# Kernel optimization log

Measured on AMD Instinct MI355X. Metric: run time of the kernel, lower is better.

The kernel has to match this reference:

```python
import jax, jax.numpy as jnp
import numpy as np

T = 3072          # num tokens
HID = 5120        # hidden_size
H = 16            # num_local_heads
DN = 128          # qk_nope_head_dim
DR = 64           # qk_rope_head_dim
DQK = DN + DR     # qk_head_dim = 192
DV = 128          # v_head_dim
Q_RANK = 1536     # q_lora_rank
KV_RANK = 512     # kv_lora_rank


def rmsnorm(x, w, eps=1e-6):
    var = jnp.mean(jnp.square(x), axis=-1, keepdims=True)
    return x * jax.lax.rsqrt(var + eps) * w


def apply_rope(x, cos, sin):
    # neox-style rotate-half; x [..., DR], cos/sin broadcastable [..., DR//2]
    x1, x2 = jnp.split(x, 2, axis=-1)
    return jnp.concatenate([x1 * cos - x2 * sin, x2 * cos + x1 * sin], axis=-1)


def setup_inputs() -> dict:
    key = jax.random.key(0)
    ks = jax.random.split(key, 8)
    s = 0.02
    positions = jnp.arange(T, dtype=jnp.int32)
    hidden_states = jax.random.normal(ks[0], (T, HID), dtype=jnp.float32)
    llama_4_scaling = jnp.ones((T, 1, 1), dtype=jnp.float32)
    w_q_a = jax.random.normal(ks[1], (HID, Q_RANK), dtype=jnp.float32) * s
    q_a_ln_w = jnp.ones((Q_RANK,), dtype=jnp.float32)
    w_q_b = jax.random.normal(ks[2], (Q_RANK, H * DQK), dtype=jnp.float32) * s
    w_kv_a = jax.random.normal(ks[3], (HID, KV_RANK + DR), dtype=jnp.float32) * s
    kv_a_ln_w = jnp.ones((KV_RANK,), dtype=jnp.float32)
    w_kv_b = jax.random.normal(ks[4], (KV_RANK, H * (DN + DV)), dtype=jnp.float32) * s
    w_o = jax.random.normal(ks[5], (H * DV, HID), dtype=jnp.float32) * s
    # cos/sin cache: [max_pos, DR]; first half cos, second half sin
    inv_freq = 1.0 / (10000.0 ** (jnp.arange(0, DR, 2, dtype=jnp.float32) / DR))
    t = jnp.arange(T, dtype=jnp.float32)
    freqs = t[:, None] * inv_freq[None, :]              # [T, DR//2]
    cos_sin_cache = jnp.concatenate([jnp.cos(freqs), jnp.sin(freqs)], axis=-1)
    return {
        "positions": positions, "hidden_states": hidden_states,
        "llama_4_scaling": llama_4_scaling,
        "w_q_a": w_q_a, "q_a_ln_w": q_a_ln_w, "w_q_b": w_q_b,
        "w_kv_a": w_kv_a, "kv_a_ln_w": kv_a_ln_w, "w_kv_b": w_kv_b,
        "w_o": w_o, "cos_sin_cache": cos_sin_cache,
    }


def reference(positions, hidden_states, llama_4_scaling, w_q_a, q_a_ln_w,
              w_q_b, w_kv_a, kv_a_ln_w, w_kv_b, w_o, cos_sin_cache):
    # ---- Q path: low-rank down/up projection with RMSNorm ----
    q = rmsnorm(hidden_states @ w_q_a, q_a_ln_w) @ w_q_b       # [T, H*DQK]
    q = q.reshape(T, H, DQK)
    q_nope, q_pe = q[..., :DN], q[..., DN:]                    # [T,H,DN],[T,H,DR]

    # ---- KV path: compressed latent + shared rope key ----
    latent = hidden_states @ w_kv_a                            # [T, KV_RANK+DR]
    kv_a = rmsnorm(latent[:, :KV_RANK], kv_a_ln_w)             # [T, KV_RANK]
    k_pe = latent[:, KV_RANK:]                                 # [T, DR] (shared across heads)
    kv = (kv_a @ w_kv_b).reshape(T, H, DN + DV)
    k_nope, v = kv[..., :DN], kv[..., DN:]                     # [T,H,DN],[T,H,DV]

    # ---- partial RoPE on the rope slices only ----
    cs = cos_sin_cache[positions]                              # [T, DR]
    cos, sin = cs[:, :DR // 2], cs[:, DR // 2:]
    q_pe = apply_rope(q_pe, cos[:, None, :], sin[:, None, :])
    k_pe = apply_rope(k_pe, cos, sin)

    q = jnp.concatenate([q_nope, q_pe], axis=-1)               # [T, H, DQK]
    k = jnp.concatenate(
        [k_nope, jnp.broadcast_to(k_pe[:, None, :], (T, H, DR))], axis=-1)

    q = q * llama_4_scaling

    # ---- causal attention (v is zero-padded to DQK in the original;
    #      the pad contributes zeros and is sliced off, so we skip it) ----
    scale = 1.0 / jnp.sqrt(jnp.float32(DQK))
    scores = jnp.einsum('qhd,khd->hqk', q, k) * scale          # [H, T, T]
    causal = positions[:, None] >= positions[None, :]
    scores = jnp.where(causal[None, :, :], scores, jnp.finfo(scores.dtype).min)
    probs = jax.nn.softmax(scores, axis=-1)
    attn = jnp.einsum('hqk,khd->qhd', probs, v)                # [T, H, DV]

    return attn.reshape(T, H * DV) @ w_o                       # [T, HID]
```

## Files before the change

### kernel.cpp

```cpp
#include <hip/hip_runtime.h>
#include <hip/hip_bf16.h>
#include <math.h>

#define T_TOK 3072
#define HID_D 5120
#define NH 16
#define DN 128
#define DR 64
#define DQK 192
#define DV 128
#define QRANK 1536
#define KVRANK 512
#define MERGED_N 2176

typedef __attribute__((ext_vector_type(8))) short short8;
typedef __attribute__((ext_vector_type(4))) float f32x4;
typedef unsigned short u16;

__device__ __forceinline__ u16 f2bf(float f) {
    unsigned int u = __float_as_uint(f);
    unsigned int lsb = (u >> 16) & 1;
    u += 0x7fffu + lsb;
    return (u16)(u >> 16);
}
__device__ __forceinline__ float bf2f(u16 v) {
    return __uint_as_float(((unsigned int)v) << 16);
}

__device__ __forceinline__ void gload_lds16(const u16* g, u16* l) {
    __builtin_amdgcn_global_load_lds((const __attribute__((address_space(1))) void*)g,
                                     (__attribute__((address_space(3))) void*)l, 16, 0, 0);
}

__global__ __launch_bounds__(256) void convert_bf_k(const float* __restrict__ x,
                                                    u16* __restrict__ y, int n4)
{
    const int i = blockIdx.x * 256 + threadIdx.x;
    if (i < n4) {
        float4 v = ((const float4*)x)[i];
        ushort4 o;
        o.x = f2bf(v.x); o.y = f2bf(v.y); o.z = f2bf(v.z); o.w = f2bf(v.w);
        ((ushort4*)y)[i] = o;
    }
}

__global__ __launch_bounds__(256) void transpose_conv_k(const float* __restrict__ W,
                                                        u16* __restrict__ WT,
                                                        int K, int N)
{
    __shared__ float tile[32][33];
    const int n0 = blockIdx.x * 32, k0 = blockIdx.y * 32;
    const int tx = threadIdx.x & 31, ty = threadIdx.x >> 5;
#pragma unroll
    for (int i = 0; i < 32; i += 8) {
        const int nn = n0 + tx;
        tile[ty + i][tx] = (nn < N) ? W[(size_t)(k0 + ty + i) * N + nn] : 0.f;
    }
    __syncthreads();
#pragma unroll
    for (int i = 0; i < 32; i += 8) {
        WT[(size_t)(n0 + ty + i) * K + k0 + tx] = f2bf(tile[tx][ty + i]);
    }
}

template <bool BF16_OUT>
__global__ __launch_bounds__(256) void bgemm_bt_k(
    const u16* __restrict__ A, const u16* __restrict__ BT, void* __restrict__ C,
    int Nreal, int K, int lda, int ldb, int ldc)
{
    __shared__ __attribute__((aligned(16))) u16 As[128 * 32];
    __shared__ __attribute__((aligned(16))) u16 Bs[128 * 32];

    const int tid  = threadIdx.x;
    const int wave = tid >> 6, lane = tid & 63;
    const int quad = lane >> 4, l16 = lane & 15;
    const int wr = (wave >> 1) * 64, wc = (wave & 1) * 64;
    const int row0 = blockIdx.y * 128, col0 = blockIdx.x * 128;

    f32x4 acc[4][4];
#pragma unroll
    for (int i = 0; i < 4; ++i)
#pragma unroll
        for (int j = 0; j < 4; ++j) acc[i][j] = (f32x4){0.f, 0.f, 0.f, 0.f};

    const int sr  = tid >> 2;
    const int skc = (tid & 3) * 8;
    const u16* ap0 = A  + (size_t)(row0 + sr)      * lda + skc;
    const u16* ap1 = A  + (size_t)(row0 + sr + 64) * lda + skc;
    const u16* bp0 = BT + (size_t)(col0 + sr)      * ldb + skc;
    const u16* bp1 = BT + (size_t)(col0 + sr + 64) * ldb + skc;
    u16* al0 = As + tid * 8;
    u16* al1 = As + tid * 8 + 64 * 32;
    u16* bl0 = Bs + tid * 8;
    u16* bl1 = Bs + tid * 8 + 64 * 32;

    for (int kt = 0; kt < K; kt += 32) {
        gload_lds16(ap0 + kt, al0);
        gload_lds16(ap1 + kt, al1);
        gload_lds16(bp0 + kt, bl0);
        gload_lds16(bp1 + kt, bl1);
        __syncthreads();

        short8 af[4], bf[4];
#pragma unroll
        for (int mi = 0; mi < 4; ++mi)
            af[mi] = *(const short8*)(As + (wr + mi * 16 + l16) * 32 + quad * 8);
#pragma unroll
        for (int ni = 0; ni < 4; ++ni)
            bf[ni] = *(const short8*)(Bs + (wc + ni * 16 + l16) * 32 + quad * 8);
#pragma unroll
        for (int mi = 0; mi < 4; ++mi)
#pragma unroll
            for (int ni = 0; ni < 4; ++ni)
                acc[mi][ni] = __builtin_amdgcn_mfma_f32_16x16x32_bf16(
                    af[mi], bf[ni], acc[mi][ni], 0, 0, 0);
        __syncthreads();
    }

#pragma unroll
    for (int mi = 0; mi < 4; ++mi) {
#pragma unroll
        for (int ni = 0; ni < 4; ++ni) {
            const int col_g = col0 + wc + ni * 16 + l16;
            if (col_g < Nreal) {
#pragma unroll
                for (int r = 0; r < 4; ++r) {
                    const int row_g = row0 + wr + mi * 16 + quad * 4 + r;
                    if (BF16_OUT)
                        ((u16*)C)[(size_t)row_g * ldc + col_g] = f2bf(acc[mi][ni][r]);
                    else
                        ((float*)C)[(size_t)row_g * ldc + col_g] = acc[mi][ni][r];
                }
            }
        }
    }
}

__global__ __launch_bounds__(256) void rmsnorm_bf_k(const u16* __restrict__ x,
                                                    const float* __restrict__ w,
                                                    u16* __restrict__ y,
                                                    int width, int stride, int off)
{
    const int row = blockIdx.x;
    const u16* xr = x + (size_t)row * stride + off;
    float ss = 0.f;
    for (int i = threadIdx.x; i < width; i += 256) {
        float v = bf2f(xr[i]);
        ss += v * v;
    }
    __shared__ float red[256];
    red[threadIdx.x] = ss;
    __syncthreads();
    for (int s = 128; s > 0; s >>= 1) {
        if (threadIdx.x < s) red[threadIdx.x] += red[threadIdx.x + s];
        __syncthreads();
    }
    const float scale = rsqrtf(red[0] / (float)width + 1e-6f);
    for (int i = threadIdx.x; i < width; i += 256)
        y[(size_t)row * width + i] = f2bf(bf2f(xr[i]) * scale * w[i]);
}

__global__ void rope_scale_q_bf_k(const u16* __restrict__ q, const int* __restrict__ positions,
                                  const float* __restrict__ scaling,
                                  const float* __restrict__ cs_cache, u16* __restrict__ qb)
{
    const int t = blockIdx.x;
    const int pos = positions[t];
    const float* cs = cs_cache + (size_t)pos * DR;
    const float s = scaling[t];
    __shared__ float c_sh[32], s_sh[32];
    if (threadIdx.x < 32) {
        c_sh[threadIdx.x] = cs[threadIdx.x];
        s_sh[threadIdx.x] = cs[32 + threadIdx.x];
    }
    __syncthreads();
    const int tid = threadIdx.x;
    for (int h = 0; h < NH; ++h) {
        const u16* qr = q + ((size_t)t * NH + h) * DQK;
        u16* qo = qb + ((size_t)t * NH + h) * DQK;
        if (tid < 128) {
            qo[tid] = f2bf(bf2f(qr[tid]) * s);
        } else if (tid < 160) {
            const int d = tid - 128;
            const float x1 = bf2f(qr[128 + d]), x2 = bf2f(qr[160 + d]);
            qo[128 + d] = f2bf((x1 * c_sh[d] - x2 * s_sh[d]) * s);
            qo[160 + d] = f2bf((x2 * c_sh[d] + x1 * s_sh[d]) * s);
        }
    }
}

__global__ void rope_k_bf_k(const u16* __restrict__ qa_lat, u16* __restrict__ kpe,
                            const int* __restrict__ positions,
                            const float* __restrict__ cs_cache)
{
    const int t = blockIdx.x;
    const int d = threadIdx.x;
    if (d >= 32) return;
    const int pos = positions[t];
    const float* cs = cs_cache + (size_t)pos * DR;
    const float c = cs[d], sn = cs[32 + d];
    const u16* lr = qa_lat + (size_t)t * MERGED_N + QRANK + KVRANK;
    const float x1 = bf2f(lr[d]), x2 = bf2f(lr[32 + d]);
    kpe[(size_t)t * DR + d]      = f2bf(x1 * c - x2 * sn);
    kpe[(size_t)t * DR + 32 + d] = f2bf(x2 * c + x1 * sn);
}

__global__ __launch_bounds__(256) void transpose_v_k(const u16* __restrict__ kvb,
                                                     u16* __restrict__ vt)
{
    __shared__ u16 tile[64][72];
    const int t0 = blockIdx.x * 64, d0 = blockIdx.y * 64, h = blockIdx.z;
    const int tid = threadIdx.x;
    for (int cc = tid; cc < 64 * 8; cc += 256) {
        const int row = cc >> 3, c = (cc & 7) * 8;
        *(short8*)&tile[row][c] =
            *(const short8*)(kvb + ((size_t)(t0 + row) * NH + h) * (DN + DV) + DN + d0 + c);
    }
    __syncthreads();
    for (int cc = tid; cc < 64 * 8; cc += 256) {
        const int drow = cc >> 3, c = (cc & 7) * 8;
        short8 s;
#pragma unroll
        for (int j = 0; j < 8; ++j) s[j] = tile[c + j][drow];
        *(short8*)(vt + ((size_t)h * DV + d0 + drow) * T_TOK + t0 + c) = s;
    }
}

#define ATT_BM 128
#define ATT_BN 64
__global__ __launch_bounds__(512) void attn_mfma_k(
    const u16* __restrict__ qb, const u16* __restrict__ kvb,
    const u16* __restrict__ kpeb, const u16* __restrict__ vt,
    u16* __restrict__ attnb)
{
    __shared__ u16 Ks[ATT_BN][200];
    __shared__ u16 Vt[DV][72];
    __shared__ u16 Ps[8][16][72];

    const int tid  = threadIdx.x;
    const int wave = tid >> 6;
    const int lane = tid & 63;
    const int quad = lane >> 4;
    const int l16  = lane & 15;

    const int qblk = (int)gridDim.x - 1 - (int)blockIdx.x;
    const int h    = blockIdx.y;
    const int q0   = qblk * ATT_BM;
    const int wrow0 = q0 + wave * 16;
    const int qrow  = wrow0 + l16;

    short8 qf[6];
    {
        const u16* qp = qb + ((size_t)qrow * NH + h) * DQK + quad * 8;
#pragma unroll
        for (int c = 0; c < 6; ++c)
            qf[c] = *(const short8*)(qp + c * 32);
    }

    f32x4 oacc[8];
#pragma unroll
    for (int t = 0; t < 8; ++t) oacc[t] = (f32x4){0.f, 0.f, 0.f, 0.f};
    float m_old[4], l_run[4];
#pragma unroll
    for (int r = 0; r < 4; ++r) { m_old[r] = -1e30f; l_run[r] = 0.f; }

    const int nkt = (q0 + ATT_BM) / ATT_BN;
    for (int kt = 0; kt < nkt; ++kt) {
        const int k0 = kt * ATT_BN;
        __syncthreads();
        for (int cc = tid; cc < 64 * 24; cc += 512) {
            const int row = cc / 24, c = cc % 24;
            short8 v;
            if (c < 16) v = *(const short8*)(kvb + ((size_t)(k0 + row) * NH + h) * (DN + DV) + c * 8);
            else        v = *(const short8*)(kpeb + (size_t)(k0 + row) * DR + (c - 16) * 8);
            *(short8*)&Ks[row][c * 8] = v;
        }
        for (int cc = tid; cc < DV * 8; cc += 512) {
            const int row = cc >> 3, c = (cc & 7) * 8;
            *(short8*)&Vt[row][c] =
                *(const short8*)(vt + ((size_t)h * DV + row) * T_TOK + k0 + c);
        }
        __syncthreads();

        if (k0 <= wrow0 + 15) {
            f32x4 sacc[4];
#pragma unroll
            for (int t = 0; t < 4; ++t) sacc[t] = (f32x4){0.f, 0.f, 0.f, 0.f};
#pragma unroll
            for (int t = 0; t < 4; ++t) {
                const u16* kp = &Ks[t * 16 + l16][quad * 8];
#pragma unroll
                for (int c = 0; c < 6; ++c) {
                    short8 bfrag = *(const short8*)(kp + c * 32);
                    sacc[t] = __builtin_amdgcn_mfma_f32_16x16x32_bf16(qf[c], bfrag, sacc[t], 0, 0, 0);
                }
            }
            const float sc = 0.07216878364870322f;
            const int rbase = wrow0 + quad * 4;
            if (k0 + ATT_BN - 1 > wrow0) {
#pragma unroll
                for (int t = 0; t < 4; ++t) {
                    const int colg = k0 + t * 16 + l16;
#pragma unroll
                    for (int r = 0; r < 4; ++r) {
                        const float s = sacc[t][r] * sc;
                        sacc[t][r] = (rbase + r >= colg) ? s : -1e30f;
                    }
                }
            } else {
#pragma unroll
                for (int t = 0; t < 4; ++t)
#pragma unroll
                    for (int r = 0; r < 4; ++r) sacc[t][r] *= sc;
            }
            float alpha[4];
#pragma unroll
            for (int r = 0; r < 4; ++r) {
                float mx = fmaxf(fmaxf(sacc[0][r], sacc[1][r]), fmaxf(sacc[2][r], sacc[3][r]));
                mx = fmaxf(mx, __shfl_xor(mx, 1));
                mx = fmaxf(mx, __shfl_xor(mx, 2));
                mx = fmaxf(mx, __shfl_xor(mx, 4));
                mx = fmaxf(mx, __shfl_xor(mx, 8));
                const float mnew = fmaxf(m_old[r], mx);
                alpha[r] = __expf(m_old[r] - mnew);
                float sum = 0.f;
#pragma unroll
                for (int t = 0; t < 4; ++t) {
                    const float p = __expf(sacc[t][r] - mnew);
                    sacc[t][r] = p;
                    sum += p;
                }
                sum += __shfl_xor(sum, 1);
                sum += __shfl_xor(sum, 2);
                sum += __shfl_xor(sum, 4);
                sum += __shfl_xor(sum, 8);
                l_run[r] = l_run[r] * alpha[r] + sum;
                m_old[r] = mnew;
            }
#pragma unroll
            for (int t = 0; t < 4; ++t)
#pragma unroll
                for (int r = 0; r < 4; ++r)
                    Ps[wave][quad * 4 + r][t * 16 + l16] = f2bf(sacc[t][r]);
#pragma unroll
            for (int t = 0; t < 8; ++t)
#pragma unroll
                for (int r = 0; r < 4; ++r)
                    oacc[t][r] *= alpha[r];
#pragma unroll
            for (int ch = 0; ch < 2; ++ch) {
                short8 pfrag = *(const short8*)&Ps[wave][l16][ch * 32 + quad * 8];
#pragma unroll
                for (int t = 0; t < 8; ++t) {
                    short8 vfrag = *(const short8*)&Vt[t * 16 + l16][ch * 32 + quad * 8];
                    oacc[t] = __builtin_amdgcn_mfma_f32_16x16x32_bf16(pfrag, vfrag, oacc[t], 0, 0, 0);
                }
            }
        }
    }

#pragma unroll
    for (int r = 0; r < 4; ++r) {
        const float linv = 1.f / l_run[r];
        const int row_g = wrow0 + quad * 4 + r;
        u16* op = attnb + (size_t)row_g * (NH * DV) + h * DV;
#pragma unroll
        for (int t = 0; t < 8; ++t)
            op[t * 16 + l16] = f2bf(oacc[t][r] * linv);
    }
}

extern "C" void kernel_launch(void* const* d_in, const int* in_sizes, int n_in,
                              void* d_out, int out_size, void* d_ws, size_t ws_size,
                              hipStream_t stream)
{
    const int*   positions = (const int*)d_in[0];
    const float* hidden    = (const float*)d_in[1];
    const float* scaling   = (const float*)d_in[2];
    const float* w_q_a     = (const float*)d_in[3];
    const float* q_a_ln_w  = (const float*)d_in[4];
    const float* w_q_b     = (const float*)d_in[5];
    const float* w_kv_a    = (const float*)d_in[6];
    const float* kv_a_ln_w = (const float*)d_in[7];
    const float* w_kv_b    = (const float*)d_in[8];
    const float* w_o       = (const float*)d_in[9];
    const float* cs_cache  = (const float*)d_in[10];
    float* out = (float*)d_out;

    char* p = (char*)d_ws;
    auto alloc = [&](size_t bytes) { char* r = p; p += (bytes + 255) & ~(size_t)255; return r; };

    char* regH      = alloc((size_t)T_TOK * HID_D * 2);
    u16*  hidden_bf = (u16*)regH;
    u16*  qraw_bf   = (u16*)regH;
    char* regQ      = alloc((size_t)T_TOK * MERGED_N * 2 + (size_t)T_TOK * QRANK * 2);
    u16*  qa_lat    = (u16*)regQ;
    u16*  q_a_norm  = (u16*)(regQ + (size_t)T_TOK * MERGED_N * 2);
    u16*  qb        = (u16*)regQ;
    u16* kv_a_norm = (u16*)alloc((size_t)T_TOK * KVRANK * 2);
    u16* kpe_bf    = (u16*)alloc((size_t)T_TOK * DR * 2);
    u16* kv_bf     = (u16*)alloc((size_t)T_TOK * NH * (DN + DV) * 2);
    u16* vt        = (u16*)alloc((size_t)NH * DV * T_TOK * 2);
    u16* attnb     = (u16*)alloc((size_t)T_TOK * NH * DV * 2);
    u16* wqakva_bt = (u16*)alloc((size_t)MERGED_N * HID_D * 2);
    u16* wqb_bt    = (u16*)alloc((size_t)(NH * DQK) * QRANK * 2);
    u16* wkvb_bt   = (u16*)alloc((size_t)(NH * (DN + DV)) * KVRANK * 2);
    u16* wo_bt     = (u16*)alloc((size_t)HID_D * (NH * DV) * 2);

    const dim3 blk(256);

    convert_bf_k<<<dim3((T_TOK * HID_D / 4 + 255) / 256), blk, 0, stream>>>(
        hidden, hidden_bf, T_TOK * HID_D / 4);
    transpose_conv_k<<<dim3(QRANK / 32, HID_D / 32), blk, 0, stream>>>(
        w_q_a, wqakva_bt, HID_D, QRANK);
    transpose_conv_k<<<dim3(640 / 32, HID_D / 32), blk, 0, stream>>>(
        w_kv_a, wqakva_bt + (size_t)QRANK * HID_D, HID_D, KVRANK + DR);
    transpose_conv_k<<<dim3(NH * DQK / 32, QRANK / 32), blk, 0, stream>>>(w_q_b, wqb_bt, QRANK, NH * DQK);
    transpose_conv_k<<<dim3(NH * (DN + DV) / 32, KVRANK / 32), blk, 0, stream>>>(w_kv_b, wkvb_bt, KVRANK, NH * (DN + DV));
    transpose_conv_k<<<dim3(HID_D / 32, NH * DV / 32), blk, 0, stream>>>(w_o, wo_bt, NH * DV, HID_D);

    bgemm_bt_k<true><<<dim3(MERGED_N / 128, T_TOK / 128), blk, 0, stream>>>(
        hidden_bf, wqakva_bt, qa_lat, QRANK + KVRANK + DR, HID_D, HID_D, HID_D, MERGED_N);
    rope_k_bf_k<<<dim3(T_TOK), dim3(64), 0, stream>>>(qa_lat, kpe_bf, positions, cs_cache);
    rmsnorm_bf_k<<<dim3(T_TOK), blk, 0, stream>>>(qa_lat, q_a_ln_w, q_a_norm, QRANK, MERGED_N, 0);
    rmsnorm_bf_k<<<dim3(T_TOK), blk, 0, stream>>>(qa_lat, kv_a_ln_w, kv_a_norm, KVRANK, MERGED_N, QRANK);
    bgemm_bt_k<true><<<dim3(NH * DQK / 128, T_TOK / 128), blk, 0, stream>>>(
        q_a_norm, wqb_bt, qraw_bf, NH * DQK, QRANK, QRANK, QRANK, NH * DQK);
    rope_scale_q_bf_k<<<dim3(T_TOK), blk, 0, stream>>>(qraw_bf, positions, scaling, cs_cache, qb);
    bgemm_bt_k<true><<<dim3(NH * (DN + DV) / 128, T_TOK / 128), blk, 0, stream>>>(
        kv_a_norm, wkvb_bt, kv_bf, NH * (DN + DV), KVRANK, KVRANK, KVRANK, NH * (DN + DV));
    transpose_v_k<<<dim3(T_TOK / 64, DV / 64, NH), blk, 0, stream>>>(kv_bf, vt);
    attn_mfma_k<<<dim3(T_TOK / ATT_BM, NH), dim3(512), 0, stream>>>(qb, kv_bf, kpe_bf, vt, attnb);
    bgemm_bt_k<false><<<dim3(HID_D / 128, T_TOK / 128), blk, 0, stream>>>(
        attnb, wo_bt, out, HID_D, NH * DV, NH * DV, NH * DV, HID_D);
}
```

Baseline: 815.9 us.

## Prefetch attention K/V tiles via registers, remap blocks, vectorize norm and rope

```diff
diff --git a/kernel.cpp b/kernel.cpp
--- a/kernel.cpp
+++ b/kernel.cpp
@@ -143,24 +143,40 @@
 {
     const int row = blockIdx.x;
     const u16* xr = x + (size_t)row * stride + off;
+    const int nch = width >> 3;
     float ss = 0.f;
-    for (int i = threadIdx.x; i < width; i += 256) {
-        float v = bf2f(xr[i]);
-        ss += v * v;
+    for (int i = threadIdx.x; i < nch; i += 256) {
+        short8 v = *(const short8*)(xr + i * 8);
+#pragma unroll
+        for (int j = 0; j < 8; ++j) { const float f = bf2f((u16)v[j]); ss += f * f; }
     }
     __shared__ float red[256];
     red[threadIdx.x] = ss;
     __syncthreads();
-    for (int s = 128; s > 0; s >>= 1) {
-        if (threadIdx.x < s) red[threadIdx.x] += red[threadIdx.x + s];
+    for (int s2 = 128; s2 > 0; s2 >>= 1) {
+        if (threadIdx.x < s2) red[threadIdx.x] += red[threadIdx.x + s2];
         __syncthreads();
     }
     const float scale = rsqrtf(red[0] / (float)width + 1e-6f);
-    for (int i = threadIdx.x; i < width; i += 256)
-        y[(size_t)row * width + i] = f2bf(bf2f(xr[i]) * scale * w[i]);
-}
-
-__global__ void rope_scale_q_bf_k(const u16* __restrict__ q, const int* __restrict__ positions,
+    u16* yr = y + (size_t)row * width;
+    for (int i = threadIdx.x; i < nch; i += 256) {
+        short8 v = *(const short8*)(xr + i * 8);
+        const float4 w0 = *(const float4*)(w + i * 8);
+        const float4 w1 = *(const float4*)(w + i * 8 + 4);
+        short8 o;
+        o[0] = (short)f2bf(bf2f((u16)v[0]) * scale * w0.x);
+        o[1] = (short)f2bf(bf2f((u16)v[1]) * scale * w0.y);
+        o[2] = (short)f2bf(bf2f((u16)v[2]) * scale * w0.z);
+        o[3] = (short)f2bf(bf2f((u16)v[3]) * scale * w0.w);
+        o[4] = (short)f2bf(bf2f((u16)v[4]) * scale * w1.x);
+        o[5] = (short)f2bf(bf2f((u16)v[5]) * scale * w1.y);
+        o[6] = (short)f2bf(bf2f((u16)v[6]) * scale * w1.z);
+        o[7] = (short)f2bf(bf2f((u16)v[7]) * scale * w1.w);
+        *(short8*)(yr + i * 8) = o;
+    }
+}
+
+__global__ __launch_bounds__(256) void rope_scale_q_bf_k(const u16* __restrict__ q, const int* __restrict__ positions,
                                   const float* __restrict__ scaling,
                                   const float* __restrict__ cs_cache, u16* __restrict__ qb)
 {
@@ -174,17 +190,32 @@
         s_sh[threadIdx.x] = cs[32 + threadIdx.x];
     }
     __syncthreads();
-    const int tid = threadIdx.x;
-    for (int h = 0; h < NH; ++h) {
-        const u16* qr = q + ((size_t)t * NH + h) * DQK;
-        u16* qo = qb + ((size_t)t * NH + h) * DQK;
-        if (tid < 128) {
-            qo[tid] = f2bf(bf2f(qr[tid]) * s);
-        } else if (tid < 160) {
-            const int d = tid - 128;
-            const float x1 = bf2f(qr[128 + d]), x2 = bf2f(qr[160 + d]);
-            qo[128 + d] = f2bf((x1 * c_sh[d] - x2 * s_sh[d]) * s);
-            qo[160 + d] = f2bf((x2 * c_sh[d] + x1 * s_sh[d]) * s);
+    const u16* qt = q + (size_t)t * NH * DQK;
+    u16* qo = qb + (size_t)t * NH * DQK;
+    for (int cc = threadIdx.x; cc < NH * 20; cc += 256) {
+        const int hh = cc / 20, c = cc % 20;
+        const u16* qr = qt + hh * DQK;
+        u16* qw = qo + hh * DQK;
+        if (c < 16) {
+            short8 v = *(const short8*)(qr + c * 8);
+            short8 o;
+#pragma unroll
+            for (int j = 0; j < 8; ++j) o[j] = (short)f2bf(bf2f((u16)v[j]) * s);
+            *(short8*)(qw + c * 8) = o;
+        } else {
+            const int d0 = (c - 16) * 8;
+            short8 x1 = *(const short8*)(qr + 128 + d0);
+            short8 x2 = *(const short8*)(qr + 160 + d0);
+            short8 o1, o2;
+#pragma unroll
+            for (int j = 0; j < 8; ++j) {
+                const float a = bf2f((u16)x1[j]), b = bf2f((u16)x2[j]);
+                const float cv = c_sh[d0 + j], sv = s_sh[d0 + j];
+                o1[j] = (short)f2bf((a * cv - b * sv) * s);
+                o2[j] = (short)f2bf((b * cv + a * sv) * s);
+            }
+            *(short8*)(qw + 128 + d0) = o1;
+            *(short8*)(qw + 160 + d0) = o2;
         }
     }
 }
@@ -228,7 +259,7 @@
 
 #define ATT_BM 128
 #define ATT_BN 64
-__global__ __launch_bounds__(512) void attn_mfma_k(
+__global__ __launch_bounds__(512, 4) void attn_mfma_k(
     const u16* __restrict__ qb, const u16* __restrict__ kvb,
     const u16* __restrict__ kpeb, const u16* __restrict__ vt,
     u16* __restrict__ attnb)
@@ -243,9 +274,12 @@
     const int quad = lane >> 4;
     const int l16  = lane & 15;
 
-    const int qblk = (int)gridDim.x - 1 - (int)blockIdx.x;
-    const int h    = blockIdx.y;
-    const int q0   = qblk * ATT_BM;
+    const int bid   = (int)blockIdx.x;
+    const int chunk = bid & 7;
+    const int local = bid >> 3;
+    const int h     = chunk * 2 + (local & 1);
+    const int qblk  = (T_TOK / ATT_BM - 1) - (local >> 1);
+    const int q0    = qblk * ATT_BM;
     const int wrow0 = q0 + wave * 16;
     const int qrow  = wrow0 + l16;
 
@@ -257,6 +291,31 @@
             qf[c] = *(const short8*)(qp + c * 32);
     }
 
+    const u16* gp[5];
+    size_t     gst[5];
+    u16*       ld[5];
+#pragma unroll
+    for (int i = 0; i < 3; ++i) {
+        const int cc = tid + 512 * i;
+        const int row = cc / 24, c = cc % 24;
+        if (c < 16) {
+            gp[i]  = kvb + ((size_t)row * NH + h) * (DN + DV) + c * 8;
+            gst[i] = (size_t)ATT_BN * NH * (DN + DV);
+        } else {
+            gp[i]  = kpeb + (size_t)row * DR + (c - 16) * 8;
+            gst[i] = (size_t)ATT_BN * DR;
+        }
+        ld[i] = &Ks[row][c * 8];
+    }
+#pragma unroll
+    for (int i = 0; i < 2; ++i) {
+        const int cc = tid + 512 * i;
+        const int row = cc >> 3, c = (cc & 7) * 8;
+        gp[3 + i]  = vt + ((size_t)h * DV + row) * T_TOK + c;
+        gst[3 + i] = (size_t)ATT_BN;
+        ld[3 + i]  = &Vt[row][c];
+    }
+
     f32x4 oacc[8];
 #pragma unroll
     for (int t = 0; t < 8; ++t) oacc[t] = (f32x4){0.f, 0.f, 0.f, 0.f};
@@ -264,24 +323,23 @@
 #pragma unroll
     for (int r = 0; r < 4; ++r) { m_old[r] = -1e30f; l_run[r] = 0.f; }
 
+    short8 streg[5];
+#pragma unroll
+    for (int i = 0; i < 5; ++i) streg[i] = *(const short8*)gp[i];
+
     const int nkt = (q0 + ATT_BM) / ATT_BN;
     for (int kt = 0; kt < nkt; ++kt) {
+        __syncthreads();
+#pragma unroll
+        for (int i = 0; i < 5; ++i) *(short8*)ld[i] = streg[i];
+        __syncthreads();
+        if (kt + 1 < nkt) {
+#pragma unroll
+            for (int i = 0; i < 5; ++i)
+                streg[i] = *(const short8*)(gp[i] + (size_t)(kt + 1) * gst[i]);
+        }
+
         const int k0 = kt * ATT_BN;
-        __syncthreads();
-        for (int cc = tid; cc < 64 * 24; cc += 512) {
-            const int row = cc / 24, c = cc % 24;
-            short8 v;
-            if (c < 16) v = *(const short8*)(kvb + ((size_t)(k0 + row) * NH + h) * (DN + DV) + c * 8);
-            else        v = *(const short8*)(kpeb + (size_t)(k0 + row) * DR + (c - 16) * 8);
-            *(short8*)&Ks[row][c * 8] = v;
-        }
-        for (int cc = tid; cc < DV * 8; cc += 512) {
-            const int row = cc >> 3, c = (cc & 7) * 8;
-            *(short8*)&Vt[row][c] =
-                *(const short8*)(vt + ((size_t)h * DV + row) * T_TOK + k0 + c);
-        }
-        __syncthreads();
-
         if (k0 <= wrow0 + 15) {
             f32x4 sacc[4];
 #pragma unroll
@@ -430,7 +488,7 @@
     bgemm_bt_k<true><<<dim3(NH * (DN + DV) / 128, T_TOK / 128), blk, 0, stream>>>(
         kv_a_norm, wkvb_bt, kv_bf, NH * (DN + DV), KVRANK, KVRANK, KVRANK, NH * (DN + DV));
     transpose_v_k<<<dim3(T_TOK / 64, DV / 64, NH), blk, 0, stream>>>(kv_bf, vt);
-    attn_mfma_k<<<dim3(T_TOK / ATT_BM, NH), dim3(512), 0, stream>>>(qb, kv_bf, kpe_bf, vt, attnb);
+    attn_mfma_k<<<dim3(T_TOK / ATT_BM * NH), dim3(512), 0, stream>>>(qb, kv_bf, kpe_bf, vt, attnb);
     bgemm_bt_k<false><<<dim3(HID_D / 128, T_TOK / 128), blk, 0, stream>>>(
         attnb, wo_bt, out, HID_D, NH * DV, NH * DV, NH * DV, HID_D);
 }
```

Result: slower. 838.3 us (+2.7%).
